# Performance work log

Measured on AMD Instinct MI355X. Metric: run time of the kernel, lower is better.

Reference implementation:

```python
import jax, jax.numpy as jnp
from jax import lax
import numpy as np

B, N, E, NA = 32, 8192, 256, 16
M_MIN, M_MAX = 3, 8192
PAD_TOKEN = -2.0
LN_EPS = 1e-3  # keras LayerNormalization default epsilon


def setup_inputs() -> dict:
    key = jax.random.key(0)
    ks = jax.random.split(key, 8)
    return {
        "x": jax.random.normal(ks[0], (B, N, E), jnp.float32),
        "mask": jnp.ones((B, N), jnp.float32),
        "barcode": jax.random.uniform(ks[1], (1, 1, E), jnp.float32),
        "Wq": 0.05 * jax.random.normal(ks[2], (E, E), jnp.float32),
        "Wk": 0.05 * jax.random.normal(ks[3], (E, E), jnp.float32),
        "Wv": 0.05 * jax.random.normal(ks[4], (E, E), jnp.float32),
        "g": jax.random.uniform(ks[5], (NA, E, E), jnp.float32, minval=-0.05, maxval=0.05),
        "w": 0.05 * jax.random.normal(ks[6], (1, NA, E, E), jnp.float32),
        "ln_gamma": jnp.ones((E,), jnp.float32),
        "ln_beta": jnp.zeros((E,), jnp.float32),
    }


def _select_one(order):
    """Greedy distance-constrained selection over a descending-sorted index list (N,).
    Matches the TF while_loop: first index always kept; a candidate is kept iff its
    abs distance to every previously kept index lies in [M_MIN, M_MAX].
    Unfilled slots stay 0 (TensorArray default)."""
    slot = jnp.arange(NA, dtype=jnp.int32)

    def body(i, state):
        sel, count = state
        cand = order[i]
        d = jnp.abs(sel - cand)
        ok = (d >= M_MIN) & (d <= M_MAX)
        active = slot < count
        valid = jnp.all(jnp.where(active, ok, True)) & (count < NA)
        sel = jnp.where((slot == count) & valid, cand, sel)
        count = count + valid.astype(jnp.int32)
        return (sel, count)

    sel0 = jnp.zeros((NA,), jnp.int32).at[0].set(order[0])
    sel, _ = lax.fori_loop(1, N, body, (sel0, jnp.int32(1)))
    return sel


def reference(x, mask, barcode, Wq, Wk, Wv, g, w, ln_gamma, ln_beta):
    m = jnp.where(mask == PAD_TOKEN, 0.0, 1.0)  # (B, N)
    bc = jnp.broadcast_to(barcode, (x.shape[0], 1, x.shape[-1]))
    q = bc @ Wq              # (B, 1, E)
    k = x @ Wk               # (B, N, E)
    v = x @ Wv               # (B, N, E)
    scale = 1.0 / jnp.sqrt(jnp.float32(x.shape[-1]))
    att = jnp.einsum('bqe,bne->bqn', q, k) * scale  # (B, 1, N)
    att = att + (1.0 - m[:, None, :]) * (-1e9)
    att = jax.nn.softmax(att, axis=-1) * m[:, None, :]
    barcode_out = jnp.einsum('bqn,bne->bqe', att, v)[:, 0, :]  # (B, E)

    att1 = att[:, 0, :]                                 # (B, N)
    order = jnp.argsort(-att1, axis=-1).astype(jnp.int32)
    inds = jnp.sort(jax.vmap(_select_one)(order), axis=-1)  # (B, NA)
    weights = jnp.take_along_axis(att1, inds, axis=1)        # (B, NA)
    outs = jnp.take_along_axis(x, inds[:, :, None], axis=1)  # (B, NA, E)

    # sinusoidal positional encoding from anchor positions
    ra = jnp.arange(E, dtype=jnp.float32) / jnp.float32(E)
    pos = jnp.sin(inds[:, :, None].astype(jnp.float32) / jnp.power(40.0, ra))
    outs = outs + pos

    # per-anchor gated projection: (B,NA,1,E) @ (NA,E,E) -> (B,NA,E)
    outs_w = jnp.einsum('bae,aef->baf', outs, w[0])
    outs_g = jax.nn.sigmoid(jnp.einsum('bae,aef->baf', outs, g))
    outs = outs_w * outs_g * weights[:, :, None]

    # LayerNorm over last axis (keras defaults: eps=1e-3, learned gamma/beta)
    mu = jnp.mean(outs, axis=-1, keepdims=True)
    var = jnp.mean(jnp.square(outs - mu), axis=-1, keepdims=True)
    outs = (outs - mu) * lax.rsqrt(var + LN_EPS) * ln_gamma + ln_beta

    return (outs, inds, weights, barcode_out)
```

## Files before the change

kernel.cpp:

```cpp
#include <hip/hip_runtime.h>

#define BB 32
#define NN 8192
#define EE 256
#define NAA 16
#define NCHUNK 16
#define CHUNK 512

#define KQ_OFF   0
#define ATT_OFF  256
#define PM_OFF   (ATT_OFF + BB*NN)
#define PL_OFF   (PM_OFF + BB*NCHUNK)
#define PS_OFF   (PL_OFF + BB*NCHUNK)
#define M_OFF    (PS_OFF + BB*NCHUNK*EE)
#define L_OFF    (M_OFF + BB)
#define INDS_OFF (L_OFF + BB)
#define WSEL_OFF (INDS_OFF + BB*NAA)

#define OUT_OUTS 0
#define OUT_INDS (BB*NAA*EE)
#define OUT_W    (OUT_INDS + BB*NAA)
#define OUT_BC   (OUT_W + BB*NAA)

__global__ __launch_bounds__(256) void prep_kernel(
    const float* __restrict__ barcode, const float* __restrict__ Wq,
    const float* __restrict__ Wk, float* __restrict__ ws) {
  __shared__ float qs[EE];
  int t = threadIdx.x;
  float acc = 0.f;
  for (int f = 0; f < EE; ++f) acc += barcode[f] * Wq[f*EE + t];
  qs[t] = acc;
  __syncthreads();
  float acc2 = 0.f;
  for (int e = 0; e < EE; ++e) acc2 += Wk[t*EE + e] * qs[e];
  ws[KQ_OFF + t] = acc2 * 0.0625f;
}

__global__ __launch_bounds__(256) void pass_a(
    const float* __restrict__ x, const float* __restrict__ mask,
    float* __restrict__ ws) {
  const int c = blockIdx.x, b = blockIdx.y;
  const int w = threadIdx.x >> 6, lane = threadIdx.x & 63;
  const float4 kq4 = ((const float4*)(ws + KQ_OFF))[lane];
  float* att = ws + ATT_OFF + (size_t)b * NN + c * CHUNK;
  const float* xb = x + ((size_t)b * NN + (size_t)c * CHUNK) * EE;
  const float* mb = mask + (size_t)b * NN + c * CHUNK;

  float m = -INFINITY, l = 0.f;
  float4 acc = {0.f, 0.f, 0.f, 0.f};
  for (int r = w; r < CHUNK; r += 4) {
    float4 xv = ((const float4*)(xb + (size_t)r * EE))[lane];
    float d = xv.x*kq4.x + xv.y*kq4.y + xv.z*kq4.z + xv.w*kq4.w;
    #pragma unroll
    for (int off = 32; off >= 1; off >>= 1) d += __shfl_xor(d, off, 64);
    float mk = mb[r];
    float a = d + ((mk == -2.0f) ? -1e9f : 0.0f);
    if (lane == 0) att[r] = a;
    float keep = (mk == -2.0f) ? 0.f : 1.f;
    if (a > m) {
      float fc = expf(m - a);
      l *= fc; acc.x *= fc; acc.y *= fc; acc.z *= fc; acc.w *= fc;
      m = a;
    }
    float p = expf(a - m) * keep;
    l += p;
    acc.x += p * xv.x; acc.y += p * xv.y; acc.z += p * xv.z; acc.w += p * xv.w;
  }
  __shared__ float sm[4], sl[4], ss[4][EE];
  ss[w][lane*4+0] = acc.x; ss[w][lane*4+1] = acc.y;
  ss[w][lane*4+2] = acc.z; ss[w][lane*4+3] = acc.w;
  if (lane == 0) { sm[w] = m; sl[w] = l; }
  __syncthreads();
  int t = threadIdx.x;
  float M = fmaxf(fmaxf(sm[0], sm[1]), fmaxf(sm[2], sm[3]));
  float f0 = expf(sm[0]-M), f1 = expf(sm[1]-M), f2 = expf(sm[2]-M), f3 = expf(sm[3]-M);
  ws[PS_OFF + (size_t)(b*NCHUNK + c)*EE + t] =
      f0*ss[0][t] + f1*ss[1][t] + f2*ss[2][t] + f3*ss[3][t];
  if (t == 0) {
    ws[PM_OFF + b*NCHUNK + c] = M;
    ws[PL_OFF + b*NCHUNK + c] = f0*sl[0] + f1*sl[1] + f2*sl[2] + f3*sl[3];
  }
}

__global__ __launch_bounds__(256) void combine_kernel(
    const float* __restrict__ Wv, float* __restrict__ ws, float* __restrict__ out) {
  int b = blockIdx.x, t = threadIdx.x;
  __shared__ float sn[EE];
  float M = -INFINITY;
  for (int c = 0; c < NCHUNK; ++c) M = fmaxf(M, ws[PM_OFF + b*NCHUNK + c]);
  float S = 0.f, L = 0.f;
  for (int c = 0; c < NCHUNK; ++c) {
    float fc = expf(ws[PM_OFF + b*NCHUNK + c] - M);
    S += fc * ws[PS_OFF + (size_t)(b*NCHUNK + c)*EE + t];
    L += fc * ws[PL_OFF + b*NCHUNK + c];
  }
  sn[t] = S / L;
  if (t == 0) { ws[M_OFF + b] = M; ws[L_OFF + b] = L; }
  __syncthreads();
  float acc = 0.f;
  for (int e = 0; e < EE; ++e) acc += sn[e] * Wv[e*EE + t];
  out[OUT_BC + b*EE + t] = acc;
}

__global__ __launch_bounds__(256) void select_kernel(
    const float* __restrict__ mask, float* __restrict__ ws, float* __restrict__ out) {
  int b = blockIdx.x, t = threadIdx.x;
  __shared__ float p[NN];
  __shared__ float bv[256];
  __shared__ int   bi[256];
  __shared__ int   sel[NAA];
  __shared__ float selw[NAA];
  const float* att = ws + ATT_OFF + (size_t)b * NN;
  float M = ws[M_OFF + b], L = ws[L_OFF + b];
  for (int n = t; n < NN; n += 256) {
    float pv = expf(att[n] - M) / L;
    if (mask[(size_t)b * NN + n] == -2.0f) pv = 0.f;
    p[n] = pv;
  }
  __syncthreads();
  for (int it = 0; it < NAA; ++it) {
    float v = -2.f; int idx = NN;
    for (int n = t; n < NN; n += 256) {
      float pv = p[n];
      if (pv > v) { v = pv; idx = n; }
    }
    bv[t] = v; bi[t] = idx;
    __syncthreads();
    for (int s = 128; s >= 1; s >>= 1) {
      if (t < s) {
        float v2 = bv[t+s]; int i2 = bi[t+s];
        if (v2 > bv[t] || (v2 == bv[t] && i2 < bi[t])) { bv[t] = v2; bi[t] = i2; }
      }
      __syncthreads();
    }
    if (t == 0) {
      int id = bi[0];
      sel[it] = id; selw[it] = bv[0];
      int lo = id - 2 < 0 ? 0 : id - 2;
      int hi = id + 2 > NN-1 ? NN-1 : id + 2;
      for (int j = lo; j <= hi; ++j) p[j] = -1.f;
    }
    __syncthreads();
  }
  if (t == 0) {
    for (int i = 1; i < NAA; ++i) {
      int ki = sel[i]; float kw = selw[i]; int j = i - 1;
      while (j >= 0 && sel[j] > ki) { sel[j+1] = sel[j]; selw[j+1] = selw[j]; --j; }
      sel[j+1] = ki; selw[j+1] = kw;
    }
  }
  __syncthreads();
  if (t < NAA) {
    out[OUT_INDS + b*NAA + t] = (float)sel[t];
    out[OUT_W    + b*NAA + t] = selw[t];
    ((int*)(ws + INDS_OFF))[b*NAA + t] = sel[t];
    ws[WSEL_OFF + b*NAA + t] = selw[t];
  }
}

__global__ __launch_bounds__(256) void final_kernel(
    const float* __restrict__ x, const float* __restrict__ g,
    const float* __restrict__ w, const float* __restrict__ ln_gamma,
    const float* __restrict__ ln_beta, const float* __restrict__ ws,
    float* __restrict__ out) {
  int a = blockIdx.x, b = blockIdx.y, f = threadIdx.x;
  __shared__ float row[EE];
  __shared__ float red[4];
  int ind = ((const int*)(ws + INDS_OFF))[b*NAA + a];
  float wt = ws[WSEL_OFF + b*NAA + a];
  float ra = (float)f / 256.0f;
  float pos = sinf((float)ind / powf(40.0f, ra));
  row[f] = x[((size_t)b * NN + ind) * EE + f] + pos;
  __syncthreads();
  const float* wa = w + (size_t)a * EE * EE;
  const float* ga = g + (size_t)a * EE * EE;
  float ow = 0.f, og = 0.f;
  for (int e = 0; e < EE; ++e) {
    float r = row[e];
    ow += r * wa[e*EE + f];
    og += r * ga[e*EE + f];
  }
  float val = ow * (1.f / (1.f + expf(-og))) * wt;
  int wv = f >> 6;
  float s = val;
  #pragma unroll
  for (int off = 32; off >= 1; off >>= 1) s += __shfl_xor(s, off, 64);
  if ((f & 63) == 0) red[wv] = s;
  __syncthreads();
  float mu = (red[0] + red[1] + red[2] + red[3]) * (1.f/256.f);
  __syncthreads();
  float dv = val - mu, sq = dv * dv;
  #pragma unroll
  for (int off = 32; off >= 1; off >>= 1) sq += __shfl_xor(sq, off, 64);
  if ((f & 63) == 0) red[wv] = sq;
  __syncthreads();
  float var = (red[0] + red[1] + red[2] + red[3]) * (1.f/256.f);
  out[OUT_OUTS + ((size_t)b * NAA + a) * EE + f] =
      dv * rsqrtf(var + 0.001f) * ln_gamma[f] + ln_beta[f];
}

extern "C" void kernel_launch(void* const* d_in, const int* in_sizes, int n_in,
                              void* d_out, int out_size, void* d_ws, size_t ws_size,
                              hipStream_t stream) {
  const float* x       = (const float*)d_in[0];
  const float* mask    = (const float*)d_in[1];
  const float* barcode = (const float*)d_in[2];
  const float* Wq      = (const float*)d_in[3];
  const float* Wk      = (const float*)d_in[4];
  const float* Wv      = (const float*)d_in[5];
  const float* g       = (const float*)d_in[6];
  const float* w       = (const float*)d_in[7];
  const float* gamma   = (const float*)d_in[8];
  const float* beta    = (const float*)d_in[9];
  float* out = (float*)d_out;
  float* ws  = (float*)d_ws;

  prep_kernel<<<1, 256, 0, stream>>>(barcode, Wq, Wk, ws);
  pass_a<<<dim3(NCHUNK, BB), 256, 0, stream>>>(x, mask, ws);
  combine_kernel<<<BB, 256, 0, stream>>>(Wv, ws, out);
  select_kernel<<<BB, 256, 0, stream>>>(mask, ws, out);
  final_kernel<<<dim3(NAA, BB), 256, 0, stream>>>(x, g, w, gamma, beta, ws, out);
}
```

Before: 514.4 us.

## Increase pass_a chunking, parallelize prep/final matvecs, use wave-shuffle argmax

Splits the streaming attention pass into 64 chunks of 128 rows instead of 16 of 512, so more blocks cover the GPU while x (256 MB) is read. prep_kernel now runs with 1024 threads, splitting the reduction dimension into four parts and using float4 loads. final_kernel splits its reduction across waves with float4 weight loads. select_kernel replaces the shared-memory tree argmax with wave shuffles. The online-softmax update becomes branchless. The cost is a larger partial-sum buffer for combine_kernel to read and some extra shared-memory reductions.

```diff
diff --git a/kernel.cpp b/kernel.cpp
--- a/kernel.cpp
+++ b/kernel.cpp
@@ -4,8 +4,8 @@
 #define NN 8192
 #define EE 256
 #define NAA 16
-#define NCHUNK 16
-#define CHUNK 512
+#define NCHUNK 64
+#define CHUNK 128
 
 #define KQ_OFF   0
 #define ATT_OFF  256
@@ -22,18 +22,34 @@
 #define OUT_W    (OUT_INDS + BB*NAA)
 #define OUT_BC   (OUT_W + BB*NAA)
 
-__global__ __launch_bounds__(256) void prep_kernel(
+__global__ __launch_bounds__(1024) void prep_kernel(
     const float* __restrict__ barcode, const float* __restrict__ Wq,
     const float* __restrict__ Wk, float* __restrict__ ws) {
+  int t = threadIdx.x & 255, q = threadIdx.x >> 8;
+  __shared__ float part[4][EE];
   __shared__ float qs[EE];
-  int t = threadIdx.x;
   float acc = 0.f;
-  for (int f = 0; f < EE; ++f) acc += barcode[f] * Wq[f*EE + t];
-  qs[t] = acc;
-  __syncthreads();
+  #pragma unroll 8
+  for (int i = 0; i < 64; ++i) {
+    int f = q * 64 + i;
+    acc += barcode[f] * Wq[f*EE + t];
+  }
+  part[q][t] = acc;
+  __syncthreads();
+  if (threadIdx.x < 256) qs[t] = part[0][t] + part[1][t] + part[2][t] + part[3][t];
+  __syncthreads();
+  const float4* wk4 = (const float4*)(Wk + (size_t)t * EE + q * 64);
+  const float4* qs4 = (const float4*)(qs + q * 64);
   float acc2 = 0.f;
-  for (int e = 0; e < EE; ++e) acc2 += Wk[t*EE + e] * qs[e];
-  ws[KQ_OFF + t] = acc2 * 0.0625f;
+  #pragma unroll
+  for (int i = 0; i < 16; ++i) {
+    float4 wv = wk4[i], qv = qs4[i];
+    acc2 += wv.x*qv.x + wv.y*qv.y + wv.z*qv.z + wv.w*qv.w;
+  }
+  part[q][t] = acc2;
+  __syncthreads();
+  if (threadIdx.x < 256)
+    ws[KQ_OFF + t] = (part[0][t] + part[1][t] + part[2][t] + part[3][t]) * 0.0625f;
 }
 
 __global__ __launch_bounds__(256) void pass_a(
@@ -57,14 +73,13 @@
     float a = d + ((mk == -2.0f) ? -1e9f : 0.0f);
     if (lane == 0) att[r] = a;
     float keep = (mk == -2.0f) ? 0.f : 1.f;
-    if (a > m) {
-      float fc = expf(m - a);
-      l *= fc; acc.x *= fc; acc.y *= fc; acc.z *= fc; acc.w *= fc;
-      m = a;
-    }
-    float p = expf(a - m) * keep;
-    l += p;
-    acc.x += p * xv.x; acc.y += p * xv.y; acc.z += p * xv.z; acc.w += p * xv.w;
+    float mn = fmaxf(m, a);
+    float fc = expf(m - mn);
+    float p  = expf(a - mn) * keep;
+    l = l * fc + p;
+    acc.x = acc.x*fc + p*xv.x; acc.y = acc.y*fc + p*xv.y;
+    acc.z = acc.z*fc + p*xv.z; acc.w = acc.w*fc + p*xv.w;
+    m = mn;
   }
   __shared__ float sm[4], sl[4], ss[4][EE];
   ss[w][lane*4+0] = acc.x; ss[w][lane*4+1] = acc.y;
@@ -98,6 +113,7 @@
   if (t == 0) { ws[M_OFF + b] = M; ws[L_OFF + b] = L; }
   __syncthreads();
   float acc = 0.f;
+  #pragma unroll 8
   for (int e = 0; e < EE; ++e) acc += sn[e] * Wv[e*EE + t];
   out[OUT_BC + b*EE + t] = acc;
 }
@@ -105,9 +121,10 @@
 __global__ __launch_bounds__(256) void select_kernel(
     const float* __restrict__ mask, float* __restrict__ ws, float* __restrict__ out) {
   int b = blockIdx.x, t = threadIdx.x;
+  int w = t >> 6, lane = t & 63;
   __shared__ float p[NN];
-  __shared__ float bv[256];
-  __shared__ int   bi[256];
+  __shared__ float wvs[4];
+  __shared__ int   wis[4];
   __shared__ int   sel[NAA];
   __shared__ float selw[NAA];
   const float* att = ws + ATT_OFF + (size_t)b * NN;
@@ -124,20 +141,24 @@
       float pv = p[n];
       if (pv > v) { v = pv; idx = n; }
     }
-    bv[t] = v; bi[t] = idx;
+    #pragma unroll
+    for (int off = 32; off >= 1; off >>= 1) {
+      float v2 = __shfl_xor(v, off, 64);
+      int   i2 = __shfl_xor(idx, off, 64);
+      if (v2 > v || (v2 == v && i2 < idx)) { v = v2; idx = i2; }
+    }
+    if (lane == 0) { wvs[w] = v; wis[w] = idx; }
     __syncthreads();
-    for (int s = 128; s >= 1; s >>= 1) {
-      if (t < s) {
-        float v2 = bv[t+s]; int i2 = bi[t+s];
-        if (v2 > bv[t] || (v2 == bv[t] && i2 < bi[t])) { bv[t] = v2; bi[t] = i2; }
+    if (t == 0) {
+      float bvv = wvs[0]; int bii = wis[0];
+      #pragma unroll
+      for (int j = 1; j < 4; ++j) {
+        float v2 = wvs[j]; int i2 = wis[j];
+        if (v2 > bvv || (v2 == bvv && i2 < bii)) { bvv = v2; bii = i2; }
       }
-      __syncthreads();
-    }
-    if (t == 0) {
-      int id = bi[0];
-      sel[it] = id; selw[it] = bv[0];
-      int lo = id - 2 < 0 ? 0 : id - 2;
-      int hi = id + 2 > NN-1 ? NN-1 : id + 2;
+      sel[it] = bii; selw[it] = bvv;
+      int lo = bii - 2 < 0 ? 0 : bii - 2;
+      int hi = bii + 2 > NN-1 ? NN-1 : bii + 2;
       for (int j = lo; j <= hi; ++j) p[j] = -1.f;
     }
     __syncthreads();
@@ -163,40 +184,52 @@
     const float* __restrict__ w, const float* __restrict__ ln_gamma,
     const float* __restrict__ ln_beta, const float* __restrict__ ws,
     float* __restrict__ out) {
-  int a = blockIdx.x, b = blockIdx.y, f = threadIdx.x;
+  int a = blockIdx.x, b = blockIdx.y, t = threadIdx.x;
   __shared__ float row[EE];
+  __shared__ float redw[4][EE];
+  __shared__ float redg[4][EE];
   __shared__ float red[4];
   int ind = ((const int*)(ws + INDS_OFF))[b*NAA + a];
   float wt = ws[WSEL_OFF + b*NAA + a];
-  float ra = (float)f / 256.0f;
+  float ra = (float)t * (1.0f/256.0f);
   float pos = sinf((float)ind / powf(40.0f, ra));
-  row[f] = x[((size_t)b * NN + ind) * EE + f] + pos;
-  __syncthreads();
-  const float* wa = w + (size_t)a * EE * EE;
-  const float* ga = g + (size_t)a * EE * EE;
-  float ow = 0.f, og = 0.f;
-  for (int e = 0; e < EE; ++e) {
+  row[t] = x[((size_t)b * NN + ind) * EE + t] + pos;
+  __syncthreads();
+  int qe = t >> 6, fq = t & 63;
+  const float4* wa4 = (const float4*)(w + (size_t)a * EE * EE);
+  const float4* ga4 = (const float4*)(g + (size_t)a * EE * EE);
+  float4 aw = {0,0,0,0}, ag = {0,0,0,0};
+  #pragma unroll 8
+  for (int i = 0; i < 64; ++i) {
+    int e = qe * 64 + i;
     float r = row[e];
-    ow += r * wa[e*EE + f];
-    og += r * ga[e*EE + f];
-  }
+    float4 wv = wa4[(size_t)e * 64 + fq];
+    float4 gv = ga4[(size_t)e * 64 + fq];
+    aw.x += r*wv.x; aw.y += r*wv.y; aw.z += r*wv.z; aw.w += r*wv.w;
+    ag.x += r*gv.x; ag.y += r*gv.y; ag.z += r*gv.z; ag.w += r*gv.w;
+  }
+  ((float4*)redw[qe])[fq] = aw;
+  ((float4*)redg[qe])[fq] = ag;
+  __syncthreads();
+  float ow = redw[0][t] + redw[1][t] + redw[2][t] + redw[3][t];
+  float og = redg[0][t] + redg[1][t] + redg[2][t] + redg[3][t];
   float val = ow * (1.f / (1.f + expf(-og))) * wt;
-  int wv = f >> 6;
+  int wv_ = t >> 6;
   float s = val;
   #pragma unroll
   for (int off = 32; off >= 1; off >>= 1) s += __shfl_xor(s, off, 64);
-  if ((f & 63) == 0) red[wv] = s;
+  if ((t & 63) == 0) red[wv_] = s;
   __syncthreads();
   float mu = (red[0] + red[1] + red[2] + red[3]) * (1.f/256.f);
   __syncthreads();
   float dv = val - mu, sq = dv * dv;
   #pragma unroll
   for (int off = 32; off >= 1; off >>= 1) sq += __shfl_xor(sq, off, 64);
-  if ((f & 63) == 0) red[wv] = sq;
+  if ((t & 63) == 0) red[wv_] = sq;
   __syncthreads();
   float var = (red[0] + red[1] + red[2] + red[3]) * (1.f/256.f);
-  out[OUT_OUTS + ((size_t)b * NAA + a) * EE + f] =
-      dv * rsqrtf(var + 0.001f) * ln_gamma[f] + ln_beta[f];
+  out[OUT_OUTS + ((size_t)b * NAA + a) * EE + t] =
+      dv * rsqrtf(var + 0.001f) * ln_gamma[t] + ln_beta[t];
 }
 
 extern "C" void kernel_launch(void* const* d_in, const int* in_sizes, int n_in,
@@ -215,7 +248,7 @@
   float* out = (float*)d_out;
   float* ws  = (float*)d_ws;
 
-  prep_kernel<<<1, 256, 0, stream>>>(barcode, Wq, Wk, ws);
+  prep_kernel<<<1, 1024, 0, stream>>>(barcode, Wq, Wk, ws);
   pass_a<<<dim3(NCHUNK, BB), 256, 0, stream>>>(x, mask, ws);
   combine_kernel<<<BB, 256, 0, stream>>>(Wv, ws, out);
   select_kernel<<<BB, 256, 0, stream>>>(mask, ws, out);
```

Measured after the change: 521.1 us. Within noise of the previous version (+1.3%).
